# Kernel tuning notes

Hardware: AMD Instinct MI355X
Metric: run time of the kernel (lower is better)

The kernel has to match this reference:

```python
import jax, jax.numpy as jnp
import numpy as np

B, TE, TD, DE, DD, U = 32, 1024, 64, 512, 512, 512
REMOVE_FACTOR = 1000000.0


def setup_inputs() -> dict:
    key = jax.random.key(0)
    k = jax.random.split(key, 7)
    return {
        "en_seq": jax.random.normal(k[0], (B, TE, DE), jnp.float32),
        "de_seq": jax.random.normal(k[1], (B, TD, DD), jnp.float32),
        "mask": jax.random.randint(k[2], (B, TE), 0, 2).astype(jnp.int32),
        # W_h is a 1x1 conv [1,1,DE,U] == dense [DE,U]; w_c is [1,1,1,U] == vector [U]
        "W_h": jax.random.normal(k[3], (DE, U), jnp.float32) / np.float32(np.sqrt(DE)),
        "W_s": jax.random.normal(k[4], (DD, U), jnp.float32) / np.float32(np.sqrt(DD)),
        "w_c": jax.random.normal(k[5], (U,), jnp.float32) * np.float32(0.05),
        "v": jax.random.normal(k[6], (U,), jnp.float32) / np.float32(np.sqrt(U)),
    }


def reference(en_seq, de_seq, mask, W_h, W_s, w_c, v):
    m_en = mask.astype(en_seq.dtype)                      # [B,TE]
    en = en_seq * m_en[:, :, None]                        # masked encoder states
    enc_feat = jnp.einsum('bte,eu->btu', en, W_h)         # 1x1 conv == dense, [B,TE,U]
    dec_feat = jnp.einsum('bsd,du->bsu', de_seq, W_s)     # [B,TD,U]
    mask_bias = (m_en - 1.0) * REMOVE_FACTOR              # masked_attention additive bias

    def step(coverage, df):
        # coverage: [B,TE]; df: [B,U]
        feat = jnp.tanh(enc_feat + df[:, None, :] + coverage[:, :, None] * w_c)  # [B,TE,U]
        mu = jnp.einsum('btu,u->bt', feat, v) + mask_bias                        # [B,TE]
        alpha = jax.nn.softmax(mu, axis=-1)                                      # [B,TE]
        ctx = jnp.einsum('bt,bte->be', alpha, en)                                # [B,DE]
        covloss = jnp.minimum(coverage, alpha)                                   # [B,TE]
        return coverage + alpha, (ctx, alpha, covloss)

    cov0 = jnp.zeros(en_seq.shape[:2], en_seq.dtype)
    _, (ctx, alphas, covlosses) = jax.lax.scan(step, cov0, jnp.swapaxes(dec_feat, 0, 1))
    ctx = jnp.swapaxes(ctx, 0, 1)                # [B,TD,DE]
    output = jnp.concatenate([de_seq, ctx], -1)  # [B,TD,DD+DE]
    return output, jnp.swapaxes(alphas, 0, 1), jnp.swapaxes(covlosses, 0, 1)
```

## Files before the change

### kernel.cpp

```cpp
#include <hip/hip_runtime.h>
#include <float.h>

#define B   32
#define TE  1024
#define TD  64
#define DE  512
#define DD  512
#define U   512
#define K   512
#define NB  8
#define RPB 128

#if __has_builtin(__builtin_amdgcn_exp2f)
#define EXP2F __builtin_amdgcn_exp2f
#else
#define EXP2F exp2f
#endif
#if __has_builtin(__builtin_amdgcn_rcpf)
#define RCPF __builtin_amdgcn_rcpf
#else
#define RCPF(x) (1.0f / (x))
#endif

#define TANH_C 2.8853900817779268f
#define L2E    1.4426950408889634f

typedef __attribute__((ext_vector_type(8))) short bf16x8;
typedef __attribute__((ext_vector_type(4))) float f32x4;


__device__ __forceinline__ float wave_reduce_sum(float v) {
    #pragma unroll
    for (int o = 32; o; o >>= 1) v += __shfl_xor(v, o, 64);
    return v;
}

__device__ __forceinline__ unsigned short f2bf(float f) {
    unsigned u = __float_as_uint(f);
    unsigned r = (u + 0x7fffu + ((u >> 16) & 1u)) >> 16;
    return (unsigned short)r;
}
__device__ __forceinline__ float bflo(unsigned x) { return __uint_as_float(x << 16); }
__device__ __forceinline__ float bfhi(unsigned x) { return __uint_as_float(x & 0xffff0000u); }
__device__ __forceinline__ void unpack8(uint4 q, float* f) {
    f[0] = bflo(q.x); f[1] = bfhi(q.x); f[2] = bflo(q.y); f[3] = bfhi(q.y);
    f[4] = bflo(q.z); f[5] = bfhi(q.z); f[6] = bflo(q.w); f[7] = bfhi(q.w);
}

__device__ __forceinline__ unsigned long long ld_agent64(const unsigned long long* p) {
    return __hip_atomic_load(p, __ATOMIC_RELAXED, __HIP_MEMORY_SCOPE_AGENT);
}
__device__ __forceinline__ void st_agent64(unsigned long long* p, unsigned long long v) {
    __hip_atomic_store(p, v, __ATOMIC_RELAXED, __HIP_MEMORY_SCOPE_AGENT);
}

#define LBAR() do { \
    asm volatile("s_waitcnt lgkmcnt(0)" ::: "memory"); \
    __builtin_amdgcn_s_barrier(); \
    __builtin_amdgcn_sched_barrier(0); \
} while (0)

__global__ __launch_bounds__(256) void k_prep(
        const float* __restrict__ en_seq, unsigned short* __restrict__ en_bf,
        const float* __restrict__ de_seq, unsigned short* __restrict__ de_bf,
        float4* __restrict__ outp,
        const float* __restrict__ W_h, unsigned short* __restrict__ Wh_t,
        const float* __restrict__ W_s, unsigned short* __restrict__ Ws_t,
        unsigned long long* __restrict__ stats)
{
    __shared__ __align__(16) unsigned char sbuf[16640];
    const int tid = threadIdx.x;
    for (int vb = blockIdx.x; vb < 3329; vb += 2048) {
        if (vb < 2176) {
            const float* src; unsigned short* dst; int rb;
            if (vb < 2048) { src = en_seq; dst = en_bf; rb = vb; }
            else           { src = de_seq; dst = de_bf; rb = vb - 2048; }
            unsigned short* tbl = (unsigned short*)sbuf;
            const float4* s4 = (const float4*)(src + (size_t)rb * 8192);
            #pragma unroll
            for (int i = 0; i < 8; i++) {
                int idx = tid + i * 256;
                float4 f = s4[idx];
                ushort4 r; r.x = f2bf(f.x); r.y = f2bf(f.y);
                r.z = f2bf(f.z); r.w = f2bf(f.w);
                *(ushort4*)&tbl[(idx >> 7) * 520 + (idx & 127) * 4] = r;
            }
            __syncthreads();
            uint4* d4 = (uint4*)(dst + (size_t)rb * 8192);
            #pragma unroll
            for (int i = 0; i < 4; i++) {
                int c = tid + i * 256;
                d4[c] = *(const uint4*)&tbl[(c & 15) * 520 + (c >> 4) * 8];
            }
            __syncthreads();
        } else if (vb < 3200) {
            size_t i = (size_t)(vb - 2176) * 256 + tid;
            size_t r = i >> 7, c = i & 127;
            outp[r * 256 + c] = ((const float4*)de_seq)[i];
        } else if (vb < 3328) {
            int id = vb - 3200;
            const float* W = (id < 64) ? W_h : W_s;
            unsigned short* Wt = (id < 64) ? Wh_t : Ws_t;
            int bid = id & 63;
            const int bx = bid & 7, by = bid >> 3;
            const int lx = tid & 63, ly = tid >> 6;
            float* t = (float*)sbuf;
            #pragma unroll
            for (int i = 0; i < 64; i += 4)
                t[(ly + i) * 65 + lx] =
                    W[(size_t)(by * 64 + ly + i) * 512 + bx * 64 + lx];
            __syncthreads();
            #pragma unroll
            for (int i = 0; i < 64; i += 4) {
                int n = bx * 64 + ly + i, k = by * 64 + lx;
                Wt[((size_t)(n >> 4) * 64 + (k >> 3)) * 128
                   + (n & 15) * 8 + (k & 7)] = f2bf(t[lx * 65 + ly + i]);
            }
            __syncthreads();
        } else {
            stats[tid] = 0ull;
            stats[tid + 256] = 0ull;
        }
    }
}

__global__ __launch_bounds__(256) void k_mfma(
        const unsigned short* __restrict__ Ae, const unsigned short* __restrict__ Be,
        unsigned short* __restrict__ Ce,
        const unsigned short* __restrict__ Ad, const unsigned short* __restrict__ Bd,
        unsigned short* __restrict__ Cd)
{
    const int tid = threadIdx.x;
    const int w = tid >> 6, lane = tid & 63;
    const int quad = lane >> 4, l16 = lane & 15;
    const short* A; const short* Bt; unsigned short* C; int mb;
    if (blockIdx.y < 256) {
        A = (const short*)Ae; Bt = (const short*)Be; C = Ce; mb = blockIdx.y * 128;
    } else {
        A = (const short*)Ad; Bt = (const short*)Bd; C = Cd; mb = (blockIdx.y - 256) * 128;
    }
    const int m0 = mb + (w >> 1) * 64;
    const int n0 = blockIdx.x * 128 + (w & 1) * 64;

    const short* Ab = A  + (size_t)(m0 >> 4) * 64 * 128 + l16 * 8;
    const short* Bb = Bt + (size_t)(n0 >> 4) * 64 * 128 + l16 * 8;

    f32x4 acc[4][4] = {};
    for (int ks = 0; ks < K; ks += 32) {
        const int kc = (ks >> 3) + quad;
        bf16x8 af[4], bg[4];
        #pragma unroll
        for (int i = 0; i < 4; i++)
            af[i] = *(const bf16x8*)(Ab + ((size_t)i * 64 + kc) * 128);
        #pragma unroll
        for (int j = 0; j < 4; j++)
            bg[j] = *(const bf16x8*)(Bb + ((size_t)j * 64 + kc) * 128);
        #pragma unroll
        for (int i = 0; i < 4; i++)
            #pragma unroll
            for (int j = 0; j < 4; j++)
                acc[i][j] = __builtin_amdgcn_mfma_f32_16x16x32_bf16(
                    af[i], bg[j], acc[i][j], 0, 0, 0);
    }
    #pragma unroll
    for (int i = 0; i < 4; i++)
        #pragma unroll
        for (int j = 0; j < 4; j++)
            #pragma unroll
            for (int r = 0; r < 4; r++) {
                int m = m0 + i * 16 + quad * 4 + r;
                int n = n0 + j * 16 + l16;
                C[(size_t)m * U + n] = f2bf(acc[i][j][r]);
            }
}

__global__ __launch_bounds__(1024, 4) void k_scan(
        const unsigned short* __restrict__ enc_bf,
        const unsigned short* __restrict__ dec_bf,
        const unsigned short* en_bf,
        const float* __restrict__ w_c,
        const float* __restrict__ v,
        const int* __restrict__ mask,
        unsigned long long* __restrict__ stats,
        float* pctx,
        float* __restrict__ out)
{
    const int blk = blockIdx.x;
    const int b = blk & 31, g = blk >> 5;
    const int tid = threadIdx.x;
    const int w = tid >> 6, lane = tid & 63;
    const int u = lane * 8;

    __shared__ __align__(16) unsigned short s_enc[RPB * U];
    __shared__ __align__(16) float s_p[RPB];
    __shared__ float  s_cov[RPB];
    __shared__ short  s_rowid[RPB];
    __shared__ unsigned long long s_bal[16];
    __shared__ float  s_wsum[16];
    __shared__ float  s_q[4][512];
    __shared__ float  s_inv;

    const int* maskb = mask + b * TE;
    float* alphas = out + (size_t)B * TD * (DD + DE);
    float* covl   = alphas + (size_t)B * TD * TE;

    float wcc[8], vv[8], vsuml;
    {
        float4 a0 = *(const float4*)&w_c[u];
        float4 a1 = *(const float4*)&w_c[u + 4];
        wcc[0]=a0.x*TANH_C; wcc[1]=a0.y*TANH_C; wcc[2]=a0.z*TANH_C; wcc[3]=a0.w*TANH_C;
        wcc[4]=a1.x*TANH_C; wcc[5]=a1.y*TANH_C; wcc[6]=a1.z*TANH_C; wcc[7]=a1.w*TANH_C;
        float4 b0 = *(const float4*)&v[u];
        float4 b1 = *(const float4*)&v[u + 4];
        vv[0]=b0.x; vv[1]=b0.y; vv[2]=b0.z; vv[3]=b0.w;
        vv[4]=b1.x; vv[5]=b1.y; vv[6]=b1.z; vv[7]=b1.w;
        vsuml = ((vv[0]+vv[1])+(vv[2]+vv[3])) + ((vv[4]+vv[5])+(vv[6]+vv[7]));
    }

    int act = (maskb[tid] != 0);
    {
        unsigned long long bal = __ballot(act);
        if (lane == 0) s_bal[w] = bal;
        if (tid < RPB) { s_p[tid] = 0.f; s_cov[tid] = 0.f; s_rowid[tid] = 0; }
        __syncthreads();
    }
    int nact = 0, pre = 0;
    {
        #pragma unroll
        for (int ww = 0; ww < 16; ww++) {
            int c = __popcll(s_bal[ww]);
            if (ww < w) pre += c;
            nact += c;
        }
        pre += __popcll(s_bal[w] & ((1ull << lane) - 1));
        if (act && (pre & 7) == g) s_rowid[pre >> 3] = (short)tid;
    }
    const int Sblk = (nact + 7 - g) >> 3;

    for (int t = tid; t < RPB * TD; t += 1024) {
        int rl = t & 127, s = t >> 7;
        if (maskb[g * RPB + rl] == 0) {
            size_t rowo = ((size_t)b * TD + s) * TE + g * RPB + rl;
            alphas[rowo] = 0.f;
            covl[rowo]   = 0.f;
        }
    }
    __syncthreads();

    {
        const int slot = tid >> 3, part = tid & 7;
        const uint4* src = (const uint4*)
            (enc_bf + ((size_t)b * TE + s_rowid[slot]) * U);
        uint4* dst = (uint4*)(s_enc + (size_t)slot * U);
        #pragma unroll
        for (int j = 0; j < 8; j++) dst[part + j * 8] = src[part + j * 8];
    }
    const int e2 = tid & 255, q4 = tid >> 8;
    unsigned enreg[32];
    {
        const unsigned* enw = (const unsigned*)en_bf;
        #pragma unroll
        for (int r = 0; r < 32; r++) {
            int rg = b * TE + s_rowid[q4 * 32 + r];
            enreg[r] = enw[((size_t)(rg >> 4) * 64 + (e2 >> 2)) * 64
                           + (rg & 15) * 4 + (e2 & 3)];
        }
    }
    float* myctx = pctx + ((size_t)b * 1024 + g * RPB) * 256;

    __syncthreads();

    uint4 qd = *(const uint4*)(dec_bf + ((size_t)b * TD) * U + u);

    float inv_prev = 0.f;
    for (int s = 0; s < TD; s++) {
        float dfc[8];
        unpack8(qd, dfc);
        #pragma unroll
        for (int j = 0; j < 8; j++) dfc[j] *= TANH_C;

        float local_esum = 0.f;
        for (int i = w; i < Sblk; i += 16) {
            float pold   = s_p[i];
            float covold = s_cov[i];
            float aprev  = pold * inv_prev;
            float cov    = covold + aprev;
            if (s > 0 && lane == 0) {
                size_t rowo = ((size_t)b * TD + (s - 1)) * TE + s_rowid[i];
                alphas[rowo] = aprev;
                covl[rowo]   = fminf(covold, aprev);
            }
            uint4 q = *(const uint4*)(s_enc + (size_t)i * U + u);
            float e[8]; unpack8(q, e);
            float acc2 = 0.f;
            #pragma unroll
            for (int j = 0; j < 8; j++) {
                float arg = fmaf(cov, wcc[j], fmaf(e[j], TANH_C, dfc[j]));
                acc2 = fmaf(vv[j], RCPF(EXP2F(arg) + 1.0f), acc2);
            }
            float part = fmaf(acc2, -2.0f, vsuml);
            part = wave_reduce_sum(part);
            float pe = EXP2F(part * L2E);
            if (lane == 0) { s_p[i] = pe; s_cov[i] = cov; }
            local_esum += pe;
        }
        if (lane == 0) s_wsum[w] = local_esum;

        LBAR();

        unsigned long long* sl = stats + ((size_t)(s & 1) * B + b) * NB;
        if (w == 0) {
            float x = (lane < 16) ? s_wsum[lane] : 0.f;
            x += __shfl_xor(x, 8, 64);
            x += __shfl_xor(x, 4, 64);
            x += __shfl_xor(x, 2, 64);
            x += __shfl_xor(x, 1, 64);
            if (lane == 0) {
                unsigned long long pv =
                    ((unsigned long long)__float_as_uint(x) << 32) |
                    (unsigned)(s + 1);
                st_agent64(&sl[g], pv);
            }
        }

        {
            int sn = (s + 1 < TD) ? s + 1 : s;
            qd = *(const uint4*)(dec_bf + (((size_t)b * TD + sn) * U + u));
        }

        {
            const float4* pb = (const float4*)&s_p[q4 * 32];
            float a0 = 0.f, a1 = 0.f;
            #pragma unroll
            for (int k = 0; k < 8; k++) {
                float4 pp = pb[k];
                a0 = fmaf(pp.x, bflo(enreg[4*k]),   a0);
                a1 = fmaf(pp.x, bfhi(enreg[4*k]),   a1);
                a0 = fmaf(pp.y, bflo(enreg[4*k+1]), a0);
                a1 = fmaf(pp.y, bfhi(enreg[4*k+1]), a1);
                a0 = fmaf(pp.z, bflo(enreg[4*k+2]), a0);
                a1 = fmaf(pp.z, bfhi(enreg[4*k+2]), a1);
                a0 = fmaf(pp.w, bflo(enreg[4*k+3]), a0);
                a1 = fmaf(pp.w, bfhi(enreg[4*k+3]), a1);
            }
            s_q[q4][2 * e2]     = a0;
            s_q[q4][2 * e2 + 1] = a1;
        }

        if (w == 0) {
            unsigned long long pv = 0;
            for (;;) {
                if (lane < NB) pv = ld_agent64(&sl[lane]);
                unsigned long long okm =
                    __ballot(lane < NB ? ((unsigned)pv == (unsigned)(s + 1)) : 1);
                if (~okm == 0ull) break;
                __builtin_amdgcn_s_sleep(1);
            }
            float tg = (lane < NB) ? __uint_as_float((unsigned)(pv >> 32)) : 0.f;
            tg = wave_reduce_sum(tg);
            if (lane == 0) s_inv = RCPF(tg);
        }

        LBAR();

        inv_prev = s_inv;

        if (tid < 512) {
            float ts = s_q[0][tid] + s_q[1][tid] + s_q[2][tid] + s_q[3][tid];
            myctx[(size_t)s * 512 + tid] = ts * inv_prev;
        }
    }

    for (int i = w; i < Sblk; i += 16) {
        if (lane == 0) {
            float aprev = s_p[i] * inv_prev;
            size_t rowo = ((size_t)b * TD + (TD - 1)) * TE + s_rowid[i];
            alphas[rowo] = aprev;
            covl[rowo]   = fminf(s_cov[i], aprev);
        }
    }
}

__global__ __launch_bounds__(1024) void k_ctx(
        const float* __restrict__ pctx, float* __restrict__ out)
{
    for (int idx = blockIdx.x * 1024 + threadIdx.x; idx < 1048576;
         idx += 256 * 1024) {
        int b = idx >> 15, rem = idx & 32767;
        const float* p = pctx + (size_t)b * 262144 + rem;
        float t = 0.f;
        #pragma unroll
        for (int g = 0; g < NB; g++) t += p[(size_t)g * 32768];
        int s = rem >> 9, e = rem & 511;
        out[((size_t)b * TD + s) * (DD + DE) + DD + e] = t;
    }
}

extern "C" void kernel_launch(void* const* d_in, const int* in_sizes, int n_in,
                              void* d_out, int out_size, void* d_ws, size_t ws_size,
                              hipStream_t stream) {
    const float* en_seq = (const float*)d_in[0];
    const float* de_seq = (const float*)d_in[1];
    const int*   mask   = (const int*)d_in[2];
    const float* W_h    = (const float*)d_in[3];
    const float* W_s    = (const float*)d_in[4];
    const float* w_c    = (const float*)d_in[5];
    const float* v      = (const float*)d_in[6];
    float* out = (float*)d_out;

    unsigned short* enc_bf = (unsigned short*)d_ws;
    unsigned short* en_bf  = enc_bf + (size_t)B * TE * U;
    unsigned short* dec_bf = en_bf  + (size_t)B * TE * DE;
    unsigned short* Wh_t   = dec_bf + (size_t)B * TD * U;
    unsigned short* de_bf  = Wh_t   + (size_t)K * U;
    unsigned short* Ws_t   = de_bf  + (size_t)B * TD * DD;
    unsigned long long* stats =
        (unsigned long long*)(Ws_t + (size_t)K * U);
    float* pctx = (float*)en_bf;

    k_prep<<<2048, 256, 0, stream>>>(en_seq, en_bf, de_seq, de_bf,
                                     (float4*)out, W_h, Wh_t, W_s, Ws_t, stats);
    k_mfma<<<dim3(4, 272), 256, 0, stream>>>(en_bf, Wh_t, enc_bf,
                                             de_bf, Ws_t, dec_bf);

    void* args[] = { (void*)&enc_bf, (void*)&dec_bf, (void*)&en_bf,
                     (void*)&w_c, (void*)&v, (void*)&mask,
                     (void*)&stats, (void*)&pctx, (void*)&out };
    hipLaunchCooperativeKernel((const void*)k_scan, dim3(256), dim3(1024),
                               args, 0, stream);

    k_ctx<<<256, 1024, 0, stream>>>(pctx, out);
}
```

Measured before the change: 514.4 us.

## Precompute next-step tanh argument bases in registers during the cross-block wait

```diff
diff --git a/kernel.cpp b/kernel.cpp
--- a/kernel.cpp
+++ b/kernel.cpp
@@ -270,39 +270,69 @@
 
     __syncthreads();
 
+    #define MAKE_BASE(bb, ii) do { \
+        const int i_ = (ii); \
+        float covs_ = s_cov[i_]; \
+        uint4 q_ = *(const uint4*)(s_enc + (size_t)i_ * U + u); \
+        float e_[8]; unpack8(q_, e_); \
+        _Pragma("unroll") \
+        for (int j = 0; j < 8; j++) \
+            (bb)[j] = fmaf(covs_, wcc[j], fmaf(e_[j], TANH_C, dfc[j])); \
+    } while (0)
+
+    #define SLOT_B(bb, ii) do { \
+        const int i_ = (ii); \
+        float pold_ = s_p[i_]; \
+        float covold_ = s_cov[i_]; \
+        float aprev_ = pold_ * inv_prev; \
+        float cov_ = covold_ + aprev_; \
+        if (s > 0 && lane == 0) { \
+            size_t rowo_ = ((size_t)b * TD + (s - 1)) * TE + s_rowid[i_]; \
+            alphas[rowo_] = aprev_; \
+            covl[rowo_]   = fminf(covold_, aprev_); \
+        } \
+        float acc2_ = 0.f; \
+        _Pragma("unroll") \
+        for (int j = 0; j < 8; j++) { \
+            float arg_ = fmaf(aprev_, wcc[j], (bb)[j]); \
+            acc2_ = fmaf(vv[j], RCPF(EXP2F(arg_) + 1.0f), acc2_); \
+        } \
+        float part_ = fmaf(acc2_, -2.0f, vsuml); \
+        part_ = wave_reduce_sum(part_); \
+        float pe_ = EXP2F(part_ * L2E); \
+        if (lane == 0) { s_p[i_] = pe_; s_cov[i_] = cov_; } \
+        local_esum += pe_; \
+    } while (0)
+
+    const int i0 = w, i1 = w + 16, i2 = w + 32, i3 = w + 48, i4 = w + 64;
+    float base0[8], base1[8], base2[8], base3[8], base4[8];
+    float dfc[8];
+
     uint4 qd = *(const uint4*)(dec_bf + ((size_t)b * TD) * U + u);
+    unpack8(qd, dfc);
+    #pragma unroll
+    for (int j = 0; j < 8; j++) dfc[j] *= TANH_C;
+    if (i0 < Sblk) MAKE_BASE(base0, i0);
+    if (i1 < Sblk) MAKE_BASE(base1, i1);
+    if (i2 < Sblk) MAKE_BASE(base2, i2);
+    if (i3 < Sblk) MAKE_BASE(base3, i3);
+    if (i4 < Sblk) MAKE_BASE(base4, i4);
 
     float inv_prev = 0.f;
     for (int s = 0; s < TD; s++) {
-        float dfc[8];
-        unpack8(qd, dfc);
-        #pragma unroll
-        for (int j = 0; j < 8; j++) dfc[j] *= TANH_C;
+        {
+            int sn = (s + 1 < TD) ? s + 1 : s;
+            qd = *(const uint4*)(dec_bf + (((size_t)b * TD + sn) * U + u));
+        }
 
         float local_esum = 0.f;
-        for (int i = w; i < Sblk; i += 16) {
-            float pold   = s_p[i];
-            float covold = s_cov[i];
-            float aprev  = pold * inv_prev;
-            float cov    = covold + aprev;
-            if (s > 0 && lane == 0) {
-                size_t rowo = ((size_t)b * TD + (s - 1)) * TE + s_rowid[i];
-                alphas[rowo] = aprev;
-                covl[rowo]   = fminf(covold, aprev);
-            }
-            uint4 q = *(const uint4*)(s_enc + (size_t)i * U + u);
-            float e[8]; unpack8(q, e);
-            float acc2 = 0.f;
-            #pragma unroll
-            for (int j = 0; j < 8; j++) {
-                float arg = fmaf(cov, wcc[j], fmaf(e[j], TANH_C, dfc[j]));
-                acc2 = fmaf(vv[j], RCPF(EXP2F(arg) + 1.0f), acc2);
-            }
-            float part = fmaf(acc2, -2.0f, vsuml);
-            part = wave_reduce_sum(part);
-            float pe = EXP2F(part * L2E);
-            if (lane == 0) { s_p[i] = pe; s_cov[i] = cov; }
-            local_esum += pe;
+        if (i0 < Sblk) SLOT_B(base0, i0);
+        if (i1 < Sblk) SLOT_B(base1, i1);
+        if (i2 < Sblk) SLOT_B(base2, i2);
+        if (i3 < Sblk) SLOT_B(base3, i3);
+        if (i4 < Sblk) SLOT_B(base4, i4);
+        for (int i = w + 80; i < Sblk; i += 16) {
+            float bt[8]; MAKE_BASE(bt, i); SLOT_B(bt, i);
         }
         if (lane == 0) s_wsum[w] = local_esum;
 
@@ -323,9 +353,15 @@
             }
         }
 
-        {
-            int sn = (s + 1 < TD) ? s + 1 : s;
-            qd = *(const uint4*)(dec_bf + (((size_t)b * TD + sn) * U + u));
+        if (s + 1 < TD) {
+            unpack8(qd, dfc);
+            #pragma unroll
+            for (int j = 0; j < 8; j++) dfc[j] *= TANH_C;
+            if (i0 < Sblk) MAKE_BASE(base0, i0);
+            if (i1 < Sblk) MAKE_BASE(base1, i1);
+            if (i2 < Sblk) MAKE_BASE(base2, i2);
+            if (i3 < Sblk) MAKE_BASE(base3, i3);
+            if (i4 < Sblk) MAKE_BASE(base4, i4);
         }
 
         {
@@ -370,6 +406,8 @@
             myctx[(size_t)s * 512 + tid] = ts * inv_prev;
         }
     }
+    #undef MAKE_BASE
+    #undef SLOT_B
 
     for (int i = w; i < Sblk; i += 16) {
         if (lane == 0) {
```

Result: slower. 1.056 ms (+105.2%).

## Fuse cross-block context reduction into scan kernel tail via flag sync

Applied to the files above, without the earlier changes.

```diff
diff --git a/kernel.cpp b/kernel.cpp
--- a/kernel.cpp
+++ b/kernel.cpp
@@ -47,6 +47,12 @@
     f[4] = bflo(q.z); f[5] = bfhi(q.z); f[6] = bflo(q.w); f[7] = bfhi(q.w);
 }
 
+__device__ __forceinline__ float ld_agent(const float* p) {
+    return __hip_atomic_load(p, __ATOMIC_RELAXED, __HIP_MEMORY_SCOPE_AGENT);
+}
+__device__ __forceinline__ void st_agent(float* p, float v) {
+    __hip_atomic_store(p, v, __ATOMIC_RELAXED, __HIP_MEMORY_SCOPE_AGENT);
+}
 __device__ __forceinline__ unsigned long long ld_agent64(const unsigned long long* p) {
     return __hip_atomic_load(p, __ATOMIC_RELAXED, __HIP_MEMORY_SCOPE_AGENT);
 }
@@ -367,7 +373,7 @@
 
         if (tid < 512) {
             float ts = s_q[0][tid] + s_q[1][tid] + s_q[2][tid] + s_q[3][tid];
-            myctx[(size_t)s * 512 + tid] = ts * inv_prev;
+            st_agent(&myctx[(size_t)s * 512 + tid], ts * inv_prev);
         }
     }
 
@@ -379,20 +385,32 @@
             covl[rowo]   = fminf(s_cov[i], aprev);
         }
     }
-}
-
-__global__ __launch_bounds__(1024) void k_ctx(
-        const float* __restrict__ pctx, float* __restrict__ out)
-{
-    for (int idx = blockIdx.x * 1024 + threadIdx.x; idx < 1048576;
-         idx += 256 * 1024) {
-        int b = idx >> 15, rem = idx & 32767;
-        const float* p = pctx + (size_t)b * 262144 + rem;
-        float t = 0.f;
-        #pragma unroll
-        for (int g = 0; g < NB; g++) t += p[(size_t)g * 32768];
-        int s = rem >> 9, e = rem & 511;
-        out[((size_t)b * TD + s) * (DD + DE) + DD + e] = t;
+
+    asm volatile("s_waitcnt vmcnt(0)" ::: "memory");
+    __syncthreads();
+    {
+        unsigned long long* sl = stats + ((size_t)(TD & 1) * B + b) * NB;
+        if (w == 0 && lane == 0)
+            st_agent64(&sl[g], (unsigned long long)(unsigned)(TD + 1));
+        if (w == 0) {
+            unsigned long long pv = 0;
+            for (;;) {
+                if (lane < NB) pv = ld_agent64(&sl[lane]);
+                unsigned long long okm =
+                    __ballot(lane < NB ? ((unsigned)pv == (unsigned)(TD + 1)) : 1);
+                if (~okm == 0ull) break;
+                __builtin_amdgcn_s_sleep(1);
+            }
+        }
+    }
+    LBAR();
+    for (int t = tid; t < 8 * 512; t += 1024) {
+        int s2 = g * 8 + (t >> 9), e = t & 511;
+        const float* pb2 = pctx + (size_t)b * 262144 + (size_t)s2 * 512 + e;
+        float ts = 0.f;
+        #pragma unroll
+        for (int g2 = 0; g2 < NB; g2++) ts += ld_agent(pb2 + (size_t)g2 * 32768);
+        out[((size_t)b * TD + s2) * (DD + DE) + DD + e] = ts;
     }
 }
 
@@ -428,6 +446,4 @@
                      (void*)&stats, (void*)&pctx, (void*)&out };
     hipLaunchCooperativeKernel((const void*)k_scan, dim3(256), dim3(1024),
                                args, 0, stream);
-
-    k_ctx<<<256, 1024, 0, stream>>>(pctx, out);
-}
+}
```

Result: no change. 524.5 us (+2.0%).
